# Performance work log

Hardware: AMD Instinct MI355X
Metric: run time of the kernel (lower is better)

Reference implementation:

```python
import jax, jax.numpy as jnp
from jax import lax
import numpy as np

L = 3          # seq_len == num_levels
B = 1
H = 180
W = 180
C = 128        # d_model
HEADS = 8
P = 4          # enc_num_points
DFF = 1024
DH = C // HEADS
HW = H * W
EPS = 1e-5


def _layer_norm(x, g, b):
    m = jnp.mean(x, axis=-1, keepdims=True)
    v = jnp.mean((x - m) ** 2, axis=-1, keepdims=True)
    return (x - m) * lax.rsqrt(v + EPS) * g + b


def _bilinear(v, x, y, h, w):
    # v: [B, heads, H*W, dh]; x, y: [B, heads, Q] in pixel coords (align_corners=False)
    x0 = jnp.floor(x)
    y0 = jnp.floor(y)
    out = jnp.zeros(v.shape[:2] + x.shape[2:] + (v.shape[-1],), v.dtype)
    for dx in (0, 1):
        for dy in (0, 1):
            cx = x0 + dx
            cy = y0 + dy
            wgt = (1.0 - jnp.abs(x - cx)) * (1.0 - jnp.abs(y - cy))
            valid = (cx >= 0) & (cx < w) & (cy >= 0) & (cy < h)
            idx = (jnp.clip(cy, 0, h - 1) * w + jnp.clip(cx, 0, w - 1)).astype(jnp.int32)
            g = jnp.take_along_axis(v, idx[..., None], axis=2)
            out = out + g * (wgt * valid.astype(v.dtype))[..., None]
    return out


def _forward(src_all, reference_points, spatial_shape, conv_w, conv_b,
             W_val, b_val, W_off, b_off, W_attn, b_attn, W_out, b_out,
             ln1_g, ln1_b, W1, b1, W2, b2, ln2_g, ln2_b):
    # ---- Query_generator: conv over cat(target, support) per temporal frame ----
    bev = jnp.transpose(src_all, (0, 1, 3, 2)).reshape(L, B, C, H, W)
    target = jnp.broadcast_to(bev[0][None], (L, B, C, H, W))
    x = jnp.concatenate([target, bev], axis=2).reshape(L * B, 2 * C, H, W)
    q = lax.conv_general_dilated(x, conv_w, (1, 1), 'SAME',
                                 dimension_numbers=('NCHW', 'OIHW', 'NCHW'))
    q = q + conv_b[None, :, None, None]
    queries = q.reshape(L, B, C, HW).transpose(0, 1, 3, 2)  # [L, B, HW, C]

    # ---- SeqMSDeformAttn ----
    key_tokens = jnp.transpose(src_all, (1, 0, 2, 3)).reshape(B, L * HW, C)
    value = (key_tokens @ W_val + b_val).reshape(B, L, HW, HEADS, DH)
    vflat = value.transpose(0, 1, 3, 2, 4)  # [B, L, heads, HW, dh]

    off = (queries @ W_off + b_off).reshape(L, B, HW, HEADS, P, 2)
    off = off.transpose(1, 2, 3, 0, 4, 5)  # [B, Lq, heads, L, P, 2]
    logits = (queries @ W_attn + b_attn).reshape(L, B, HW, HEADS, P)
    logits = logits.transpose(1, 2, 3, 0, 4)  # [B, Lq, heads, L, P]
    attn = jax.nn.softmax(logits.reshape(B, HW, HEADS, L * P), axis=-1)
    attn = attn.reshape(B, HW, HEADS, L, P)

    # offset normalizer = (W_l, H_l); locations normalized to [0,1]
    normalizer = spatial_shape[:, ::-1].astype(jnp.float32)  # [L, 2]
    locs = reference_points[:, :, None, :, None, :] + off / normalizer[None, None, None, :, None, :]

    out = jnp.zeros((B, HW, HEADS, DH), jnp.float32)
    for l in range(L):
        px = locs[:, :, :, l, :, 0] * W - 0.5  # [B, Lq, heads, P]
        py = locs[:, :, :, l, :, 1] * H - 0.5
        px = px.transpose(0, 2, 1, 3).reshape(B, HEADS, HW * P)
        py = py.transpose(0, 2, 1, 3).reshape(B, HEADS, HW * P)
        samp = _bilinear(vflat[:, l], px, py, H, W).reshape(B, HEADS, HW, P, DH)
        out = out + jnp.einsum('bhqpd,bqhp->bqhd', samp, attn[:, :, :, l, :])

    src2 = out.reshape(B, HW, C) @ W_out + b_out

    # ---- residual + norm + FFN (dropout = 0) ----
    src = _layer_norm(src_all[0] + src2, ln1_g, ln1_b)
    ffn = jax.nn.relu(src @ W1 + b1) @ W2 + b2
    return _layer_norm(src + ffn, ln2_g, ln2_b)


def setup_inputs() -> dict:
    key = jax.random.key(0)
    ks = jax.random.split(key, 12)
    s = 0.02
    return {
        'src_all': jax.random.normal(ks[0], (L, B, HW, C), jnp.float32),
        'reference_points': jax.random.uniform(ks[1], (B, HW, L, 2), dtype=jnp.float32),
        'spatial_shape': jnp.full((L, 2), 180, dtype=jnp.int32),
        'conv_w': jax.random.normal(ks[2], (C, 2 * C, 3, 3), jnp.float32) * s,
        'conv_b': jnp.zeros((C,), jnp.float32),
        'W_val': jax.random.normal(ks[3], (C, C), jnp.float32) * s,
        'b_val': jnp.zeros((C,), jnp.float32),
        'W_off': jax.random.normal(ks[4], (C, HEADS * P * 2), jnp.float32) * s,
        'b_off': jax.random.normal(ks[5], (HEADS * P * 2,), jnp.float32) * 0.1,
        'W_attn': jax.random.normal(ks[6], (C, HEADS * P), jnp.float32) * s,
        'b_attn': jnp.zeros((HEADS * P,), jnp.float32),
        'W_out': jax.random.normal(ks[7], (C, C), jnp.float32) * s,
        'b_out': jnp.zeros((C,), jnp.float32),
        'ln1_g': jnp.ones((C,), jnp.float32),
        'ln1_b': jnp.zeros((C,), jnp.float32),
        'W1': jax.random.normal(ks[8], (C, DFF), jnp.float32) * s,
        'b1': jnp.zeros((DFF,), jnp.float32),
        'W2': jax.random.normal(ks[9], (DFF, C), jnp.float32) * s,
        'b2': jnp.zeros((C,), jnp.float32),
        'ln2_g': jnp.ones((C,), jnp.float32),
        'ln2_b': jnp.zeros((C,), jnp.float32),
    }


def reference(src_all, reference_points, spatial_shape, conv_w, conv_b,
              W_val, b_val, W_off, b_off, W_attn, b_attn, W_out, b_out,
              ln1_g, ln1_b, W1, b1, W2, b2, ln2_g, ln2_b):
    return _forward(src_all, reference_points, spatial_shape, conv_w, conv_b,
                    W_val, b_val, W_off, b_off, W_attn, b_attn, W_out, b_out,
                    ln1_g, ln1_b, W1, b1, W2, b2, ln2_g, ln2_b)
```

## Files before the change

### kernel.cpp

```cpp
#include <hip/hip_runtime.h>

typedef unsigned short u16;
typedef unsigned int u32;

#define HDIM 180
#define HW 32400
#define CC 128

#define CAN_SRC   0
#define CAN_REF   12441600
#define CAN_CW    12636000
#define CAN_CB    12930912
#define CAN_WVAL  12931040
#define CAN_BVAL  12947424
#define CAN_WOFF  12947552
#define CAN_BOFF  12955744
#define CAN_WATTN 12955808
#define CAN_BATTN 12959904
#define CAN_WOUT  12959936
#define CAN_BOUT  12976320
#define CAN_LN1G  12976448
#define CAN_LN1B  12976576
#define CAN_W1    12976704
#define CAN_B1    13107776
#define CAN_W2    13108800
#define CAN_B2    13239872
#define CAN_LN2G  13240000
#define CAN_LN2B  13240128
#define CAN_TOTAL 13240256

typedef short short8 __attribute__((ext_vector_type(8)));
typedef float f32x4v __attribute__((ext_vector_type(4)));

__device__ __forceinline__ float bf2f(u16 v) { return __uint_as_float(((u32)v) << 16); }
__device__ __forceinline__ u16 f2bf(float f) {
    u32 x = __float_as_uint(f);
    return (u16)((x + 0x7FFFu + ((x >> 16) & 1u)) >> 16);
}
__device__ __forceinline__ void bf8_to_f(const uint4 v, float* o) {
    o[0] = __uint_as_float(v.x << 16); o[1] = __uint_as_float(v.x & 0xFFFF0000u);
    o[2] = __uint_as_float(v.y << 16); o[3] = __uint_as_float(v.y & 0xFFFF0000u);
    o[4] = __uint_as_float(v.z << 16); o[5] = __uint_as_float(v.z & 0xFFFF0000u);
    o[6] = __uint_as_float(v.w << 16); o[7] = __uint_as_float(v.w & 0xFFFF0000u);
}

struct PtrsZ { const void* p[20]; };

__global__ __launch_bounds__(256) void convert_z(PtrsZ ptrs, u16* __restrict__ out)
{
    const int offs[20] = {CAN_SRC, CAN_REF, CAN_CW, CAN_CB, CAN_WVAL, CAN_BVAL,
                          CAN_WOFF, CAN_BOFF, CAN_WATTN, CAN_BATTN, CAN_WOUT, CAN_BOUT,
                          CAN_LN1G, CAN_LN1B, CAN_W1, CAN_B1, CAN_W2, CAN_B2,
                          CAN_LN2G, CAN_LN2B};
    int gid = blockIdx.x * 256 + threadIdx.x;
    if (gid >= CAN_TOTAL) return;
    int t = 0;
    #pragma unroll
    for (int i = 1; i < 20; i++) t += (gid >= offs[i]) ? 1 : 0;
    int e = gid - offs[t];
    bool isb = (*(const u32*)ptrs.p[12]) == 0x3F803F80u;
    out[gid] = isb ? ((const u16*)ptrs.p[t])[e] : f2bf(((const float*)ptrs.p[t])[e]);
}

__global__ __launch_bounds__(256) void prep1_z(
    const u16* __restrict__ cw, const u16* __restrict__ wval, const u16* __restrict__ wout,
    const u16* __restrict__ woff, const u16* __restrict__ wattn,
    const u16* __restrict__ boff, const u16* __restrict__ battn,
    u16* __restrict__ wtbuf, u16* __restrict__ wvalT,
    u16* __restrict__ wcat, u16* __restrict__ b128, u16* __restrict__ woutT)
{
    int gid = blockIdx.x * 256 + threadIdx.x;
    if (gid < 294912) {
        int ci = gid & 127, co = (gid >> 7) & 127, rest = gid >> 14;
        int tap = rest % 9, half = rest / 9;
        wtbuf[gid] = cw[(size_t)co * 2304 + (half * 128 + ci) * 9 + tap];
    } else if (gid < 311296) {
        int e = gid - 294912;
        int k = e >> 7, n = e & 127;
        wvalT[n * 128 + k] = wval[e];
    } else if (gid < 327808) {
        int e = gid - 311296;
        if (e < 16384) {
            int n = e >> 7, k = e & 127;
            u16 v = 0;
            if (n < 64) v = woff[k * 64 + n];
            else if (n < 96) v = wattn[k * 32 + (n - 64)];
            wcat[n * 128 + k] = v;
        } else {
            int n = e - 16384;
            u16 v = 0;
            if (n < 64) v = boff[n]; else if (n < 96) v = battn[n - 64];
            b128[n] = v;
        }
    } else if (gid < 344192) {
        int e = gid - 327808;
        int k = e >> 7, n = e & 127;
        woutT[n * 128 + k] = wout[e];
    }
}

__global__ __launch_bounds__(256) void w12t_z(
    const u16* __restrict__ w1, const u16* __restrict__ w2,
    u16* __restrict__ w1t, u16* __restrict__ w2t)
{
    int gid = blockIdx.x * 256 + threadIdx.x;
    if (gid < 131072) {
        int k = gid >> 10, n = gid & 1023;
        w1t[(size_t)n * 128 + k] = w1[gid];
    } else if (gid < 262144) {
        int e = gid - 131072;
        int k = e >> 7, n = e & 127;
        w2t[(size_t)n * 1024 + k] = w2[e];
    }
}

template<bool OUT_BF16, bool RELU, bool RES>
__global__ __launch_bounds__(256) void gemm_z(
    const u16* __restrict__ A, const u16* __restrict__ W, const u16* __restrict__ bias,
    void* __restrict__ outp, const u16* __restrict__ res, int M, int N, int K)
{
    __shared__ float As[64][68];
    __shared__ float Bs[64][68];
    const int tid = threadIdx.x;
    const int tx = tid & 15, ty = tid >> 4;
    const int m0 = blockIdx.y * 64, n0 = blockIdx.x * 64;
    float acc[4][4] = {};

    for (int k0 = 0; k0 < K; k0 += 64) {
        __syncthreads();
        #pragma unroll
        for (int i = tid; i < 512; i += 256) {
            int row = i >> 3, part = i & 7;
            float f[8];
            if (m0 + row < M) {
                uint4 v = *(const uint4*)(A + (size_t)(m0 + row) * K + k0 + part * 8);
                bf8_to_f(v, f);
            } else {
                #pragma unroll
                for (int j = 0; j < 8; j++) f[j] = 0.f;
            }
            #pragma unroll
            for (int j = 0; j < 8; j++) As[part * 8 + j][row] = f[j];
        }
        #pragma unroll
        for (int i = tid; i < 512; i += 256) {
            int kr = i >> 3, np = i & 7;
            float f[8];
            uint4 v = *(const uint4*)(W + (size_t)(k0 + kr) * N + n0 + np * 8);
            bf8_to_f(v, f);
            #pragma unroll
            for (int j = 0; j < 8; j++) Bs[kr][np * 8 + j] = f[j];
        }
        __syncthreads();
        #pragma unroll 8
        for (int kk = 0; kk < 64; kk++) {
            float4 a = *(const float4*)&As[kk][ty * 4];
            float4 b = *(const float4*)&Bs[kk][tx * 4];
            float av[4] = {a.x, a.y, a.z, a.w};
            float bv[4] = {b.x, b.y, b.z, b.w};
            #pragma unroll
            for (int i = 0; i < 4; i++)
                #pragma unroll
                for (int j = 0; j < 4; j++)
                    acc[i][j] += av[i] * bv[j];
        }
    }

    #pragma unroll
    for (int i = 0; i < 4; i++) {
        int row = m0 + ty * 4 + i;
        if (row >= M) continue;
        #pragma unroll
        for (int j = 0; j < 4; j++) {
            int col = n0 + tx * 4 + j;
            float v = acc[i][j] + bf2f(bias[col]);
            if (RELU) v = v > 0.f ? v : 0.f;
            if (RES) v += bf2f(res[(size_t)row * N + col]);
            if (OUT_BF16) ((u16*)outp)[(size_t)row * N + col] = f2bf(v);
            else          ((float*)outp)[(size_t)row * N + col] = v;
        }
    }
}

__global__ __launch_bounds__(256) void conv_z(
    const u16* __restrict__ src, const u16* __restrict__ cw, const u16* __restrict__ cb,
    u16* __restrict__ queries)
{
    __shared__ float in_lds[8 * 6 * 22];
    __shared__ float w_lds[8 * 9 * 128];
    const int tid = threadIdx.x;
    const int wt = blockIdx.x, ht = blockIdx.y, l = blockIdx.z;
    const int h0 = ht * 4, w0 = wt * 20;
    const int cog = tid & 15, pxg = tid >> 4;
    const int pr = pxg >> 2, c0 = (pxg & 3) * 5;

    float acc[5][8] = {};

    for (int ch = 0; ch < 32; ch++) {
        const int ci0 = ch * 8;
        const int fsel = (ci0 < 128) ? 0 : l;
        const int cbase = ci0 & 127;
        __syncthreads();
        if (tid < 132) {
            int r = tid / 22, c = tid % 22;
            int gh = h0 - 1 + r, gw = w0 - 1 + c;
            float f[8];
            if (gh >= 0 && gh < HDIM && gw >= 0 && gw < HDIM) {
                uint4 v = *(const uint4*)(src + ((size_t)fsel * HW + gh * HDIM + gw) * CC + cbase);
                bf8_to_f(v, f);
            } else {
                #pragma unroll
                for (int j = 0; j < 8; j++) f[j] = 0.f;
            }
            #pragma unroll
            for (int j = 0; j < 8; j++) in_lds[j * 132 + r * 22 + c] = f[j];
        }
        for (int i = tid; i < 1152; i += 256) {
            int co = i & 127, part = i >> 7;
            uint4 v = *(const uint4*)(cw + (size_t)co * 2304 + ci0 * 9 + part * 8);
            float f[8]; bf8_to_f(v, f);
            #pragma unroll
            for (int j = 0; j < 8; j++) {
                int flat = part * 8 + j;
                int ci = flat / 9, k = flat % 9;
                w_lds[ci * 1152 + k * 128 + co] = f[j];
            }
        }
        __syncthreads();

        #pragma unroll
        for (int ci = 0; ci < 8; ci++) {
            float xv[3][7];
            #pragma unroll
            for (int r = 0; r < 3; r++)
                #pragma unroll
                for (int c = 0; c < 7; c++)
                    xv[r][c] = in_lds[ci * 132 + (pr + r) * 22 + (c0 + c)];
            const float* wbase = &w_lds[ci * 1152];
            #pragma unroll
            for (int j8 = 0; j8 < 8; j8++) {
                int co = cog + 16 * j8;
                float w_[9];
                #pragma unroll
                for (int k = 0; k < 9; k++) w_[k] = wbase[k * 128 + co];
                #pragma unroll
                for (int j = 0; j < 5; j++) {
                    acc[j][j8] += xv[0][j] * w_[0] + xv[0][j + 1] * w_[1] + xv[0][j + 2] * w_[2]
                                + xv[1][j] * w_[3] + xv[1][j + 1] * w_[4] + xv[1][j + 2] * w_[5]
                                + xv[2][j] * w_[6] + xv[2][j + 1] * w_[7] + xv[2][j + 2] * w_[8];
                }
            }
        }
    }

    float bias[8];
    #pragma unroll
    for (int j8 = 0; j8 < 8; j8++) bias[j8] = bf2f(cb[cog + 16 * j8]);
    #pragma unroll
    for (int j = 0; j < 5; j++) {
        int q = (h0 + pr) * HDIM + (w0 + c0 + j);
        u16* qp = queries + ((size_t)l * HW + q) * CC;
        #pragma unroll
        for (int j8 = 0; j8 < 8; j8++)
            qp[cog + 16 * j8] = f2bf(acc[j][j8] + bias[j8]);
    }
}

template<int MODE>
__global__ __launch_bounds__(256) void convh_z(
    const u16* __restrict__ src, const u16* __restrict__ wt, const u16* __restrict__ cb,
    f32x4v* __restrict__ q0, u16* __restrict__ queries)
{
    __shared__ uint4 Blds[2][2048];
    const int tid = threadIdx.x;
    const int wv = tid >> 6, ln = tid & 63;
    const int lo = ln & 15, hi = ln >> 4;
    const int l = (MODE == 1) ? blockIdx.y : 0;
    const int pix0 = blockIdx.x * 128 + wv * 32;
    const int pb0 = blockIdx.x * 8 + wv * 2;

    int ph[2], pc[2];
    #pragma unroll
    for (int s = 0; s < 2; s++) {
        int p = pix0 + s * 16 + lo;
        ph[s] = p / HDIM; pc[s] = p % HDIM;
    }

    f32x4v acc[2][8];
    if (MODE == 0) {
        #pragma unroll
        for (int s = 0; s < 2; s++)
            #pragma unroll
            for (int c = 0; c < 8; c++) acc[s][c] = (f32x4v){0.f, 0.f, 0.f, 0.f};
    } else {
        #pragma unroll
        for (int s = 0; s < 2; s++)
            #pragma unroll
            for (int c = 0; c < 8; c++)
                acc[s][c] = q0[((size_t)(pb0 + s) * 8 + c) * 64 + ln];
    }

    const u16* wthalf = wt + (MODE == 1 ? (size_t)9 * 16384 : 0);
    const u16* sbase  = src + (MODE == 1 ? (size_t)l * HW * CC : 0);

    const int sco = tid >> 1, spart = tid & 1;
    const int sc8 = sco >> 4, slo = sco & 15;

    {
        const uint4* g = (const uint4*)(wthalf + (size_t)sco * 128 + spart * 64);
        uint4 gr[8];
        #pragma unroll
        for (int i = 0; i < 8; i++) gr[i] = g[i];
        #pragma unroll
        for (int i = 0; i < 8; i++) {
            int k8 = spart * 8 + i;
            Blds[0][((k8 >> 2) * 8 + sc8) * 64 + (k8 & 3) * 16 + slo] = gr[i];
        }
    }
    __syncthreads();

    for (int t = 0; t < 9; t++) {
        const int cur = t & 1;

        uint4 gr[8];
        if (t < 8) {
            const uint4* g = (const uint4*)(wthalf + (size_t)(t + 1) * 16384 +
                                            (size_t)sco * 128 + spart * 64);
            #pragma unroll
            for (int i = 0; i < 8; i++) gr[i] = g[i];
        }

        const int dy = t / 3 - 1, dx = t % 3 - 1;
        const int sh0 = ph[0] + dy, sc0 = pc[0] + dx;
        const int sh1 = ph[1] + dy, sc1 = pc[1] + dx;
        const bool v0 = (sh0 >= 0) && (sh0 < HDIM) && (sc0 >= 0) && (sc0 < HDIM);
        const bool v1 = (sh1 >= 0) && (sh1 < HDIM) && (sc1 >= 0) && (sc1 < HDIM);
        const u16* arow0 = sbase + (size_t)(sh0 * HDIM + sc0) * CC;
        const u16* arow1 = sbase + (size_t)(sh1 * HDIM + sc1) * CC;

        #pragma unroll
        for (int kc = 0; kc < 4; kc++) {
            short8 a0 = {}, a1 = {};
            if (v0) a0 = *(const short8*)(arow0 + kc * 32 + hi * 8);
            if (v1) a1 = *(const short8*)(arow1 + kc * 32 + hi * 8);
            #pragma unroll
            for (int c = 0; c < 8; c++) {
                short8 b = ((const short8*)&Blds[cur][0])[(kc * 8 + c) * 64 + ln];
                acc[0][c] = __builtin_amdgcn_mfma_f32_16x16x32_bf16(a0, b, acc[0][c], 0, 0, 0);
                acc[1][c] = __builtin_amdgcn_mfma_f32_16x16x32_bf16(a1, b, acc[1][c], 0, 0, 0);
            }
        }

        if (t < 8) {
            #pragma unroll
            for (int i = 0; i < 8; i++) {
                int k8 = spart * 8 + i;
                Blds[cur ^ 1][((k8 >> 2) * 8 + sc8) * 64 + (k8 & 3) * 16 + slo] = gr[i];
            }
        }
        __syncthreads();
    }

    if (MODE == 0) {
        #pragma unroll
        for (int s = 0; s < 2; s++)
            #pragma unroll
            for (int c = 0; c < 8; c++)
                q0[((size_t)(pb0 + s) * 8 + c) * 64 + ln] = acc[s][c];
    } else {
        #pragma unroll
        for (int s = 0; s < 2; s++) {
            #pragma unroll
            for (int c = 0; c < 8; c++) {
                float bv = bf2f(cb[c * 16 + lo]);
                #pragma unroll
                for (int r = 0; r < 4; r++) {
                    int pr = pix0 + s * 16 + hi * 4 + r;
                    if (pr < HW)
                        queries[((size_t)l * HW + pr) * CC + c * 16 + lo] =
                            f2bf(acc[s][c][r] + bv);
                }
            }
        }
    }
}

template<int OMODE, bool RELU, bool RES, bool LN>
__global__ __launch_bounds__(256) void gemmm_z(
    const u16* __restrict__ A, const u16* __restrict__ WT, const u16* __restrict__ bias,
    void* __restrict__ outp, const u16* __restrict__ res,
    const u16* __restrict__ lng, const u16* __restrict__ lnb,
    int M, int K, int ldc, int ncols)
{
    __shared__ u16 Blds[128 * 136];
    const int tid = threadIdx.x;
    const int wv = tid >> 6, ln = tid & 63;
    const int lo = ln & 15, hi = ln >> 4;
    const int m0 = blockIdx.y * 64, n0 = blockIdx.x * 128;
    const int row = m0 + wv * 16 + lo;
    const u16* arow = A + (size_t)row * K;

    f32x4v acc[8] = {};

    for (int ks = 0; ks < K; ks += 128) {
        __syncthreads();
        {
            int n = tid >> 1, part = tid & 1;
            const uint4* g = (const uint4*)(WT + (size_t)(n0 + n) * K + ks + part * 64);
            uint4* d = (uint4*)&Blds[n * 136 + part * 64];
            #pragma unroll
            for (int i = 0; i < 8; i++) d[i] = g[i];
        }
        __syncthreads();
        #pragma unroll
        for (int kc = 0; kc < 4; kc++) {
            short8 a = *(const short8*)(arow + ks + kc * 32 + hi * 8);
            #pragma unroll
            for (int c = 0; c < 8; c++) {
                short8 b = *(const short8*)&Blds[(c * 16 + lo) * 136 + kc * 32 + hi * 8];
                acc[c] = __builtin_amdgcn_mfma_f32_16x16x32_bf16(a, b, acc[c], 0, 0, 0);
            }
        }
    }

    #pragma unroll
    for (int r = 0; r < 4; r++) {
        int orow = m0 + wv * 16 + hi * 4 + r;
        if (orow >= M) continue;
        float vv[8];
        #pragma unroll
        for (int c = 0; c < 8; c++) {
            int col = n0 + c * 16 + lo;
            float v = 0.f;
            if (col < ncols) {
                v = acc[c][r] + bf2f(bias[col]);
                if (RELU) v = v > 0.f ? v : 0.f;
                if (RES) v += bf2f(res[(size_t)orow * ldc + col]);
            }
            vv[c] = v;
        }
        if (LN) {
            float s1 = 0.f;
            #pragma unroll
            for (int c = 0; c < 8; c++) s1 += vv[c];
            #pragma unroll
            for (int o = 8; o; o >>= 1) s1 += __shfl_xor(s1, o, 64);
            float mean = s1 * (1.f / 128.f);
            float s2 = 0.f;
            #pragma unroll
            for (int c = 0; c < 8; c++) { float d = vv[c] - mean; s2 += d * d; }
            #pragma unroll
            for (int o = 8; o; o >>= 1) s2 += __shfl_xor(s2, o, 64);
            float rr = rsqrtf(s2 * (1.f / 128.f) + 1e-5f);
            #pragma unroll
            for (int c = 0; c < 8; c++) {
                int col = n0 + c * 16 + lo;
                vv[c] = (vv[c] - mean) * rr * bf2f(lng[col]) + bf2f(lnb[col]);
            }
        }
        #pragma unroll
        for (int c = 0; c < 8; c++) {
            int col = n0 + c * 16 + lo;
            if (col >= ncols) continue;
            if (OMODE == 0)
                ((float*)outp)[(size_t)orow * ldc + col] = vv[c];
            else
                ((u16*)outp)[(size_t)orow * ldc + col] = f2bf(vv[c]);
        }
    }
}

__global__ __launch_bounds__(256, 4) void sample3_z(
    const u16* __restrict__ value, const float* __restrict__ proj,
    const float* __restrict__ ref, u16* __restrict__ outp)
{
    const int tid = threadIdx.x;
    const int q = blockIdx.x * 16 + (tid >> 4);
    const int head = tid & 7;
    const int phv = (tid >> 3) & 1;
    if (q >= HW) return;

    float lg[12];
    #pragma unroll
    for (int l = 0; l < 3; l++) {
        float4 v = *(const float4*)(proj + (size_t)(l * HW + q) * 96 + 64 + head * 4);
        lg[l * 4 + 0] = v.x; lg[l * 4 + 1] = v.y; lg[l * 4 + 2] = v.z; lg[l * 4 + 3] = v.w;
    }
    float m = lg[0];
    #pragma unroll
    for (int i = 1; i < 12; i++) m = fmaxf(m, lg[i]);
    float w12[12], sum = 0.f;
    #pragma unroll
    for (int i = 0; i < 12; i++) { w12[i] = __expf(lg[i] - m); sum += w12[i]; }
    float inv = 1.f / sum;

    float acc[16] = {};
    #pragma unroll
    for (int l = 0; l < 3; l++) {
        float rx = ref[(size_t)(q * 3 + l) * 2 + 0] * 180.f - 0.5f;
        float ry = ref[(size_t)(q * 3 + l) * 2 + 1] * 180.f - 0.5f;
        float4 o = *(const float4*)(proj + (size_t)(l * HW + q) * 96 + head * 8 + phv * 4);
        float ox[2] = {o.x, o.z};
        float oy[2] = {o.y, o.w};
        #pragma unroll
        for (int pp = 0; pp < 2; pp++) {
            int p = phv * 2 + pp;
            float px = rx + ox[pp];
            float py = ry + oy[pp];
            float x0f = floorf(px), y0f = floorf(py);
            int x0 = (int)x0f, y0 = (int)y0f;
            float fx = px - x0f, fy = py - y0f;
            float a = w12[l * 4 + p] * inv;
            #pragma unroll
            for (int dy = 0; dy < 2; dy++) {
                int cy = y0 + dy;
                float wy = (dy ? fy : 1.f - fy) * a;
                wy = (cy >= 0 && cy < HDIM) ? wy : 0.f;
                int cyc = min(max(cy, 0), HDIM - 1);
                #pragma unroll
                for (int dx = 0; dx < 2; dx++) {
                    int cx = x0 + dx;
                    float wq = (dx ? fx : 1.f - fx) * wy;
                    wq = (cx >= 0 && cx < HDIM) ? wq : 0.f;
                    int cxc = min(max(cx, 0), HDIM - 1);
                    const uint4* vp = (const uint4*)(value +
                        (((size_t)l * HW + cyc * HDIM + cxc) * CC + head * 16));
                    uint4 va = vp[0], vb = vp[1];
                    float f[8];
                    bf8_to_f(va, f);
                    #pragma unroll
                    for (int d = 0; d < 8; d++) acc[d] += wq * f[d];
                    bf8_to_f(vb, f);
                    #pragma unroll
                    for (int d = 0; d < 8; d++) acc[8 + d] += wq * f[d];
                }
            }
        }
    }
    #pragma unroll
    for (int d = 0; d < 16; d++) acc[d] += __shfl_xor(acc[d], 8, 64);
    if (phv == 0) {
        u16 pack[16];
        #pragma unroll
        for (int d = 0; d < 16; d++) pack[d] = f2bf(acc[d]);
        uint4* op = (uint4*)(outp + (size_t)q * CC + head * 16);
        op[0] = ((uint4*)pack)[0];
        op[1] = ((uint4*)pack)[1];
    }
}

__global__ __launch_bounds__(256) void sample_z(
    const u16* __restrict__ value, const u16* __restrict__ queries,
    const u16* __restrict__ woff, const u16* __restrict__ boff,
    const u16* __restrict__ wattn, const u16* __restrict__ battn,
    const float* __restrict__ ref, u16* __restrict__ outp)
{
    __shared__ u16 w_lds[128 * 96];
    __shared__ float bias_lds[96];
    const int tid = threadIdx.x;

    for (int i = tid; i < 128 * 96; i += 256) {
        int k = i / 96, c = i % 96;
        w_lds[i] = (c < 64) ? woff[k * 64 + c] : wattn[k * 32 + (c - 64)];
    }
    if (tid < 96) bias_lds[tid] = bf2f(tid < 64 ? boff[tid] : battn[tid - 64]);
    __syncthreads();

    int q = blockIdx.x * 32 + (tid >> 3);
    int head = tid & 7;
    if (q >= HW) return;

    float og[3][8], lg[12];
    #pragma unroll
    for (int l = 0; l < 3; l++) {
        const u16* qr = queries + ((size_t)l * HW + q) * CC;
        float a12[12] = {};
        #pragma unroll
        for (int kc = 0; kc < 16; kc++) {
            float f[8];
            bf8_to_f(*(const uint4*)(qr + kc * 8), f);
            #pragma unroll
            for (int j = 0; j < 8; j++) {
                const u16* wr = &w_lds[(kc * 8 + j) * 96];
                #pragma unroll
                for (int c = 0; c < 8; c++) a12[c] += f[j] * bf2f(wr[head * 8 + c]);
                #pragma unroll
                for (int c = 0; c < 4; c++) a12[8 + c] += f[j] * bf2f(wr[64 + head * 4 + c]);
            }
        }
        #pragma unroll
        for (int c = 0; c < 8; c++) og[l][c] = a12[c] + bias_lds[head * 8 + c];
        #pragma unroll
        for (int c = 0; c < 4; c++) lg[l * 4 + c] = a12[8 + c] + bias_lds[64 + head * 4 + c];
    }

    float m = lg[0];
    #pragma unroll
    for (int i = 1; i < 12; i++) m = fmaxf(m, lg[i]);
    float w12[12], sum = 0.f;
    #pragma unroll
    for (int i = 0; i < 12; i++) { w12[i] = __expf(lg[i] - m); sum += w12[i]; }
    float inv = 1.f / sum;

    float acc[16] = {};
    #pragma unroll
    for (int l = 0; l < 3; l++) {
        float rx = ref[(size_t)(q * 3 + l) * 2 + 0];
        float ry = ref[(size_t)(q * 3 + l) * 2 + 1];
        #pragma unroll
        for (int p = 0; p < 4; p++) {
            float px = rx * 180.f + og[l][p * 2 + 0] - 0.5f;
            float py = ry * 180.f + og[l][p * 2 + 1] - 0.5f;
            float x0f = floorf(px), y0f = floorf(py);
            int x0 = (int)x0f, y0 = (int)y0f;
            float fx = px - x0f, fy = py - y0f;
            float a = w12[l * 4 + p] * inv;
            #pragma unroll
            for (int dy = 0; dy < 2; dy++) {
                int cy = y0 + dy;
                if (cy < 0 || cy >= HDIM) continue;
                #pragma unroll
                for (int dx = 0; dx < 2; dx++) {
                    int cx = x0 + dx;
                    if (cx < 0 || cx >= HDIM) continue;
                    float wq = a * ((dx ? fx : 1.f - fx) * (dy ? fy : 1.f - fy));
                    const uint4* vp = (const uint4*)(value + (((size_t)l * HW + cy * HDIM + cx) * CC + head * 16));
                    uint4 va = vp[0], vb = vp[1];
                    float f[8];
                    bf8_to_f(va, f);
                    #pragma unroll
                    for (int d = 0; d < 8; d++) acc[d] += wq * f[d];
                    bf8_to_f(vb, f);
                    #pragma unroll
                    for (int d = 0; d < 8; d++) acc[8 + d] += wq * f[d];
                }
            }
        }
    }
    u16 pack[16];
    #pragma unroll
    for (int d = 0; d < 16; d++) pack[d] = f2bf(acc[d]);
    uint4* op = (uint4*)(outp + (size_t)q * CC + head * 16);
    op[0] = ((uint4*)pack)[0];
    op[1] = ((uint4*)pack)[1];
}

__global__ __launch_bounds__(256) void ln_z(
    u16* __restrict__ x, const u16* __restrict__ g, const u16* __restrict__ b, int M)
{
    int row = blockIdx.x * 4 + (threadIdx.x >> 6);
    int lane = threadIdx.x & 63;
    if (row >= M) return;
    u16* xr = x + (size_t)row * 128;
    float v0 = bf2f(xr[lane]), v1 = bf2f(xr[lane + 64]);
    float s = v0 + v1;
    #pragma unroll
    for (int o = 32; o; o >>= 1) s += __shfl_xor(s, o, 64);
    float mean = s * (1.f / 128.f);
    float d0 = v0 - mean, d1 = v1 - mean;
    float vs = d0 * d0 + d1 * d1;
    #pragma unroll
    for (int o = 32; o; o >>= 1) vs += __shfl_xor(vs, o, 64);
    float r = rsqrtf(vs * (1.f / 128.f) + 1e-5f);
    xr[lane]      = f2bf(d0 * r * bf2f(g[lane])      + bf2f(b[lane]));
    xr[lane + 64] = f2bf(d1 * r * bf2f(g[lane + 64]) + bf2f(b[lane + 64]));
}

__global__ __launch_bounds__(256) void ln32_z(
    float* __restrict__ x, const u16* __restrict__ g, const u16* __restrict__ b, int M)
{
    int row = blockIdx.x * 4 + (threadIdx.x >> 6);
    int lane = threadIdx.x & 63;
    if (row >= M) return;
    float* xr = x + (size_t)row * 128;
    float v0 = xr[lane], v1 = xr[lane + 64];
    float s = v0 + v1;
    #pragma unroll
    for (int o = 32; o; o >>= 1) s += __shfl_xor(s, o, 64);
    float mean = s * (1.f / 128.f);
    float d0 = v0 - mean, d1 = v1 - mean;
    float vs = d0 * d0 + d1 * d1;
    #pragma unroll
    for (int o = 32; o; o >>= 1) vs += __shfl_xor(vs, o, 64);
    float r = rsqrtf(vs * (1.f / 128.f) + 1e-5f);
    xr[lane]      = d0 * r * bf2f(g[lane])      + bf2f(b[lane]);
    xr[lane + 64] = d1 * r * bf2f(g[lane + 64]) + bf2f(b[lane + 64]);
}

extern "C" void kernel_launch(void* const* d_in, const int* in_sizes, int n_in,
                              void* d_out, int out_size, void* d_ws, size_t ws_size,
                              hipStream_t stream)
{
    char* ws = (char*)d_ws;
    u16* canon   = (u16*)ws;
    u16* value   = (u16*)(ws + 26480512);
    u16* queries = (u16*)(ws + 51363712);
    u16* src     = (u16*)(ws + 26480512);
    float* dout  = (float*)d_out;

    const size_t PROJ_OFF = 76246912;
    const size_t PROJ_END = PROJ_OFF + (size_t)3 * HW * 96 * 4;
    const bool big = ws_size >= PROJ_END;
    float* proj  = (float*)(ws + PROJ_OFF);
    u16* wtbuf   = (u16*)(ws + PROJ_OFF);
    f32x4v* q0   = (f32x4v*)(ws + PROJ_OFF + 1048576);
    u16* out_s   = big ? (u16*)(ws + 51363712) : (u16*)(ws + 76246912);
    u16* hidden  = (u16*)(ws + 51363712);

    u16* WvalT = (u16*)(ws + 51363712);
    u16* W1T   = (u16*)(ws + 34774912);
    u16* W2T   = (u16*)(ws + 35037056);
    u16* wcatT = (u16*)d_out;
    u16* b128  = (u16*)d_out + 16384;
    u16* WoutT = (u16*)d_out + 32768;

    int i_cw = 2;
    while (i_cw < n_in - 17 && in_sizes[i_cw] != 294912) i_cw++;
    if (i_cw >= n_in - 17) i_cw = 3;

    PtrsZ ptrs;
    ptrs.p[0] = d_in[0];
    ptrs.p[1] = d_in[1];
    for (int i = 0; i < 18; i++) ptrs.p[2 + i] = d_in[i_cw + i];

    const u16* csrc  = canon + CAN_SRC;
    const u16* ccw   = canon + CAN_CW;
    const u16* ccb   = canon + CAN_CB;
    const u16* cWval = canon + CAN_WVAL,  *cbval = canon + CAN_BVAL;
    const u16* cWoff = canon + CAN_WOFF,  *cboff = canon + CAN_BOFF;
    const u16* cWatt = canon + CAN_WATTN, *cbatt = canon + CAN_BATTN;
    const u16* cWout = canon + CAN_WOUT,  *cbout = canon + CAN_BOUT;
    const u16* cg1   = canon + CAN_LN1G,  *cb1n  = canon + CAN_LN1B;
    const u16* cW1   = canon + CAN_W1,    *cbf1  = canon + CAN_B1;
    const u16* cW2   = canon + CAN_W2,    *cbf2  = canon + CAN_B2;
    const u16* cg2   = canon + CAN_LN2G,  *cb2n  = canon + CAN_LN2B;

    convert_z<<<dim3((CAN_TOTAL + 255) / 256), 256, 0, stream>>>(ptrs, canon);

    const int M3 = 3 * HW, M1 = HW;

    if (big) {
        prep1_z<<<dim3((344192 + 255) / 256), 256, 0, stream>>>(
            ccw, cWval, cWout, cWoff, cWatt, cboff, cbatt,
            wtbuf, WvalT, wcatT, b128, WoutT);
        gemmm_z<1, false, false, false><<<dim3(1, 1519), 256, 0, stream>>>(
            csrc, WvalT, cbval, value, nullptr, nullptr, nullptr, M3, 128, 128, 128);
        convh_z<0><<<dim3((HW + 127) / 128, 1), 256, 0, stream>>>(
            csrc, wtbuf, ccb, q0, queries);
        convh_z<1><<<dim3((HW + 127) / 128, 3), 256, 0, stream>>>(
            csrc, wtbuf, ccb, q0, queries);
        gemmm_z<0, false, false, false><<<dim3(1, 1519), 256, 0, stream>>>(
            queries, wcatT, b128, proj, nullptr, nullptr, nullptr, M3, 128, 96, 96);
        sample3_z<<<dim3((HW + 15) / 16), 256, 0, stream>>>(
            value, proj, (const float*)d_in[1], out_s);
        w12t_z<<<dim3(1024), 256, 0, stream>>>(cW1, cW2, W1T, W2T);
        gemmm_z<1, false, true, true><<<dim3(1, 507), 256, 0, stream>>>(
            out_s, WoutT, cbout, src, csrc, cg1, cb1n, M1, 128, 128, 128);
        for (int sblk = 0; sblk < 2; sblk++) {
            const u16* srow = src + (size_t)sblk * 16200 * 128;
            float* drow = dout + (size_t)sblk * 16200 * 128;
            gemmm_z<1, true, false, false><<<dim3(8, 254), 256, 0, stream>>>(
                srow, W1T, cbf1, hidden, nullptr, nullptr, nullptr, 16200, 128, 1024, 1024);
            gemmm_z<0, false, true, true><<<dim3(1, 254), 256, 0, stream>>>(
                hidden, W2T, cbf2, drow, srow, cg2, cb2n, 16200, 1024, 128, 128);
        }
    } else {
        u16* out_f = (u16*)(ws + 76246912);
        u16* hid_f = (u16*)(ws + 51363712);
        gemm_z<true, false, false><<<dim3(2, 1519), 256, 0, stream>>>(
            csrc, cWval, cbval, value, nullptr, M3, 128, 128);
        conv_z<<<dim3(9, 45, 3), 256, 0, stream>>>(csrc, ccw, ccb, queries);
        sample_z<<<dim3(1013), 256, 0, stream>>>(
            value, queries, cWoff, cboff, cWatt, cbatt, (const float*)d_in[1], out_f);
        gemm_z<true, false, true><<<dim3(2, 507), 256, 0, stream>>>(
            out_f, cWout, cbout, src, csrc, M1, 128, 128);
        ln_z<<<dim3(8100), 256, 0, stream>>>(src, cg1, cb1n, M1);
        for (int sblk = 0; sblk < 4; sblk++) {
            const u16* srow = src + (size_t)sblk * 8100 * 128;
            float* drow = dout + (size_t)sblk * 8100 * 128;
            gemm_z<true, true, false><<<dim3(16, 127), 256, 0, stream>>>(
                srow, cW1, cbf1, hid_f, nullptr, 8100, 1024, 128);
            gemm_z<false, false, true><<<dim3(2, 127), 256, 0, stream>>>(
                hid_f, cW2, cbf2, drow, srow, 8100, 128, 1024);
        }
        ln32_z<<<dim3(8100), 256, 0, stream>>>(dout, cg2, cb2n, M1);
    }
}
```

Before: 597.5 us.

## Fold offset/attention projection weights into the query conv weights

Precomputes the product of the 3x3 conv weights with the concatenated offset/attention projection matrix, plus a folded bias, so the conv kernels write the 96-wide projection directly. This removes the separate projection GEMM and the bf16 queries intermediate, and narrows the conv output from 128 to 96 channels. In exchange it adds a small weight-fold kernel that runs every call, and it changes rounding because the folded weights are stored in bf16.

```diff
diff --git a/kernel.cpp b/kernel.cpp
--- a/kernel.cpp
+++ b/kernel.cpp
@@ -63,39 +63,44 @@
 }
 
 __global__ __launch_bounds__(256) void prep1_z(
-    const u16* __restrict__ cw, const u16* __restrict__ wval, const u16* __restrict__ wout,
-    const u16* __restrict__ woff, const u16* __restrict__ wattn,
-    const u16* __restrict__ boff, const u16* __restrict__ battn,
-    u16* __restrict__ wtbuf, u16* __restrict__ wvalT,
-    u16* __restrict__ wcat, u16* __restrict__ b128, u16* __restrict__ woutT)
+    const u16* __restrict__ wval, const u16* __restrict__ wout,
+    u16* __restrict__ wvalT, u16* __restrict__ woutT)
 {
     int gid = blockIdx.x * 256 + threadIdx.x;
-    if (gid < 294912) {
-        int ci = gid & 127, co = (gid >> 7) & 127, rest = gid >> 14;
-        int tap = rest % 9, half = rest / 9;
-        wtbuf[gid] = cw[(size_t)co * 2304 + (half * 128 + ci) * 9 + tap];
-    } else if (gid < 311296) {
-        int e = gid - 294912;
-        int k = e >> 7, n = e & 127;
-        wvalT[n * 128 + k] = wval[e];
-    } else if (gid < 327808) {
-        int e = gid - 311296;
-        if (e < 16384) {
-            int n = e >> 7, k = e & 127;
-            u16 v = 0;
-            if (n < 64) v = woff[k * 64 + n];
-            else if (n < 96) v = wattn[k * 32 + (n - 64)];
-            wcat[n * 128 + k] = v;
-        } else {
-            int n = e - 16384;
-            u16 v = 0;
-            if (n < 64) v = boff[n]; else if (n < 96) v = battn[n - 64];
-            b128[n] = v;
-        }
-    } else if (gid < 344192) {
-        int e = gid - 327808;
+    if (gid < 16384) {
+        int k = gid >> 7, n = gid & 127;
+        wvalT[n * 128 + k] = wval[gid];
+    } else if (gid < 32768) {
+        int e = gid - 16384;
         int k = e >> 7, n = e & 127;
         woutT[n * 128 + k] = wout[e];
+    }
+}
+
+__global__ __launch_bounds__(256) void wfold_z(
+    const u16* __restrict__ cw, const u16* __restrict__ woff, const u16* __restrict__ wattn,
+    const u16* __restrict__ boff, const u16* __restrict__ battn, const u16* __restrict__ cb,
+    u16* __restrict__ wf, float* __restrict__ pb)
+{
+    int gid = blockIdx.x * 256 + threadIdx.x;
+    if (gid < 221184) {
+        int ci = gid & 127;
+        int n  = (gid >> 7) % 96;
+        int rest = gid / 12288;
+        int t = rest % 9, h = rest / 9;
+        float acc = 0.f;
+        for (int co = 0; co < 128; co++) {
+            float wc  = bf2f(cw[(size_t)co * 2304 + (h * 128 + ci) * 9 + t]);
+            float cat = bf2f(n < 64 ? woff[co * 64 + n] : wattn[co * 32 + (n - 64)]);
+            acc += wc * cat;
+        }
+        wf[((size_t)(h * 9 + t) * 96 + n) * 128 + ci] = f2bf(acc);
+    } else if (gid < 221280) {
+        int n = gid - 221184;
+        float acc = bf2f(n < 64 ? boff[n] : battn[n - 64]);
+        for (int k = 0; k < 128; k++)
+            acc += bf2f(cb[k]) * bf2f(n < 64 ? woff[k * 64 + n] : wattn[k * 32 + (n - 64)]);
+        pb[n] = acc;
     }
 }
 
@@ -268,10 +273,10 @@
 
 template<int MODE>
 __global__ __launch_bounds__(256) void convh_z(
-    const u16* __restrict__ src, const u16* __restrict__ wt, const u16* __restrict__ cb,
-    f32x4v* __restrict__ q0, u16* __restrict__ queries)
-{
-    __shared__ uint4 Blds[2][2048];
+    const u16* __restrict__ src, const u16* __restrict__ wf, const float* __restrict__ pb,
+    f32x4v* __restrict__ p0, float* __restrict__ proj)
+{
+    __shared__ uint4 Blds[2][1536];
     const int tid = threadIdx.x;
     const int wv = tid >> 6, ln = tid & 63;
     const int lo = ln & 15, hi = ln >> 4;
@@ -286,35 +291,35 @@
         ph[s] = p / HDIM; pc[s] = p % HDIM;
     }
 
-    f32x4v acc[2][8];
+    f32x4v acc[2][6];
     if (MODE == 0) {
         #pragma unroll
         for (int s = 0; s < 2; s++)
             #pragma unroll
-            for (int c = 0; c < 8; c++) acc[s][c] = (f32x4v){0.f, 0.f, 0.f, 0.f};
+            for (int c = 0; c < 6; c++) acc[s][c] = (f32x4v){0.f, 0.f, 0.f, 0.f};
     } else {
         #pragma unroll
         for (int s = 0; s < 2; s++)
             #pragma unroll
-            for (int c = 0; c < 8; c++)
-                acc[s][c] = q0[((size_t)(pb0 + s) * 8 + c) * 64 + ln];
-    }
-
-    const u16* wthalf = wt + (MODE == 1 ? (size_t)9 * 16384 : 0);
+            for (int c = 0; c < 6; c++)
+                acc[s][c] = p0[((size_t)(pb0 + s) * 6 + c) * 64 + ln];
+    }
+
+    const u16* wfhalf = wf + (MODE == 1 ? (size_t)9 * 12288 : 0);
     const u16* sbase  = src + (MODE == 1 ? (size_t)l * HW * CC : 0);
 
-    const int sco = tid >> 1, spart = tid & 1;
-    const int sc8 = sco >> 4, slo = sco & 15;
-
-    {
-        const uint4* g = (const uint4*)(wthalf + (size_t)sco * 128 + spart * 64);
+    const int sn = tid >> 1, spart = tid & 1;
+    const int sc6 = sn >> 4, slo = sn & 15;
+
+    if (tid < 192) {
+        const uint4* g = (const uint4*)(wfhalf + (size_t)sn * 128 + spart * 64);
         uint4 gr[8];
         #pragma unroll
         for (int i = 0; i < 8; i++) gr[i] = g[i];
         #pragma unroll
         for (int i = 0; i < 8; i++) {
             int k8 = spart * 8 + i;
-            Blds[0][((k8 >> 2) * 8 + sc8) * 64 + (k8 & 3) * 16 + slo] = gr[i];
+            Blds[0][((k8 >> 2) * 6 + sc6) * 64 + (k8 & 3) * 16 + slo] = gr[i];
         }
     }
     __syncthreads();
@@ -323,9 +328,9 @@
         const int cur = t & 1;
 
         uint4 gr[8];
-        if (t < 8) {
-            const uint4* g = (const uint4*)(wthalf + (size_t)(t + 1) * 16384 +
-                                            (size_t)sco * 128 + spart * 64);
+        if (t < 8 && tid < 192) {
+            const uint4* g = (const uint4*)(wfhalf + (size_t)(t + 1) * 12288 +
+                                            (size_t)sn * 128 + spart * 64);
             #pragma unroll
             for (int i = 0; i < 8; i++) gr[i] = g[i];
         }
@@ -344,18 +349,18 @@
             if (v0) a0 = *(const short8*)(arow0 + kc * 32 + hi * 8);
             if (v1) a1 = *(const short8*)(arow1 + kc * 32 + hi * 8);
             #pragma unroll
-            for (int c = 0; c < 8; c++) {
-                short8 b = ((const short8*)&Blds[cur][0])[(kc * 8 + c) * 64 + ln];
+            for (int c = 0; c < 6; c++) {
+                short8 b = ((const short8*)&Blds[cur][0])[(kc * 6 + c) * 64 + ln];
                 acc[0][c] = __builtin_amdgcn_mfma_f32_16x16x32_bf16(a0, b, acc[0][c], 0, 0, 0);
                 acc[1][c] = __builtin_amdgcn_mfma_f32_16x16x32_bf16(a1, b, acc[1][c], 0, 0, 0);
             }
         }
 
-        if (t < 8) {
+        if (t < 8 && tid < 192) {
             #pragma unroll
             for (int i = 0; i < 8; i++) {
                 int k8 = spart * 8 + i;
-                Blds[cur ^ 1][((k8 >> 2) * 8 + sc8) * 64 + (k8 & 3) * 16 + slo] = gr[i];
+                Blds[cur ^ 1][((k8 >> 2) * 6 + sc6) * 64 + (k8 & 3) * 16 + slo] = gr[i];
             }
         }
         __syncthreads();
@@ -365,20 +370,19 @@
         #pragma unroll
         for (int s = 0; s < 2; s++)
             #pragma unroll
-            for (int c = 0; c < 8; c++)
-                q0[((size_t)(pb0 + s) * 8 + c) * 64 + ln] = acc[s][c];
+            for (int c = 0; c < 6; c++)
+                p0[((size_t)(pb0 + s) * 6 + c) * 64 + ln] = acc[s][c];
     } else {
         #pragma unroll
         for (int s = 0; s < 2; s++) {
             #pragma unroll
-            for (int c = 0; c < 8; c++) {
-                float bv = bf2f(cb[c * 16 + lo]);
+            for (int c = 0; c < 6; c++) {
+                float bv = pb[c * 16 + lo];
                 #pragma unroll
                 for (int r = 0; r < 4; r++) {
                     int pr = pix0 + s * 16 + hi * 4 + r;
                     if (pr < HW)
-                        queries[((size_t)l * HW + pr) * CC + c * 16 + lo] =
-                            f2bf(acc[s][c][r] + bv);
+                        proj[((size_t)l * HW + pr) * 96 + c * 16 + lo] = acc[s][c][r] + bv;
                 }
             }
         }
@@ -694,7 +698,6 @@
     char* ws = (char*)d_ws;
     u16* canon   = (u16*)ws;
     u16* value   = (u16*)(ws + 26480512);
-    u16* queries = (u16*)(ws + 51363712);
     u16* src     = (u16*)(ws + 26480512);
     float* dout  = (float*)d_out;
 
@@ -702,17 +705,17 @@
     const size_t PROJ_END = PROJ_OFF + (size_t)3 * HW * 96 * 4;
     const bool big = ws_size >= PROJ_END;
     float* proj  = (float*)(ws + PROJ_OFF);
-    u16* wtbuf   = (u16*)(ws + PROJ_OFF);
-    f32x4v* q0   = (f32x4v*)(ws + PROJ_OFF + 1048576);
-    u16* out_s   = big ? (u16*)(ws + 51363712) : (u16*)(ws + 76246912);
+
+    u16* WvalT = (u16*)(ws + 51363712);
+    u16* wfold = (u16*)(ws + 51363712 + 65536);
+    f32x4v* p0 = (f32x4v*)(ws + 51363712 + 1048576);
+    u16* out_s   = (u16*)(ws + 51363712);
     u16* hidden  = (u16*)(ws + 51363712);
 
-    u16* WvalT = (u16*)(ws + 51363712);
     u16* W1T   = (u16*)(ws + 34774912);
     u16* W2T   = (u16*)(ws + 35037056);
-    u16* wcatT = (u16*)d_out;
-    u16* b128  = (u16*)d_out + 16384;
-    u16* WoutT = (u16*)d_out + 32768;
+    u16* WoutT = (u16*)d_out;
+    float* pbv = (float*)((u16*)d_out + 32768);
 
     int i_cw = 2;
     while (i_cw < n_in - 17 && in_sizes[i_cw] != 294912) i_cw++;
@@ -740,17 +743,15 @@
     const int M3 = 3 * HW, M1 = HW;
 
     if (big) {
-        prep1_z<<<dim3((344192 + 255) / 256), 256, 0, stream>>>(
-            ccw, cWval, cWout, cWoff, cWatt, cboff, cbatt,
-            wtbuf, WvalT, wcatT, b128, WoutT);
+        prep1_z<<<dim3(128), 256, 0, stream>>>(cWval, cWout, WvalT, WoutT);
+        wfold_z<<<dim3((221280 + 255) / 256), 256, 0, stream>>>(
+            ccw, cWoff, cWatt, cboff, cbatt, ccb, wfold, pbv);
         gemmm_z<1, false, false, false><<<dim3(1, 1519), 256, 0, stream>>>(
             csrc, WvalT, cbval, value, nullptr, nullptr, nullptr, M3, 128, 128, 128);
         convh_z<0><<<dim3((HW + 127) / 128, 1), 256, 0, stream>>>(
-            csrc, wtbuf, ccb, q0, queries);
+            csrc, wfold, pbv, p0, proj);
         convh_z<1><<<dim3((HW + 127) / 128, 3), 256, 0, stream>>>(
-            csrc, wtbuf, ccb, q0, queries);
-        gemmm_z<0, false, false, false><<<dim3(1, 1519), 256, 0, stream>>>(
-            queries, wcatT, b128, proj, nullptr, nullptr, nullptr, M3, 128, 96, 96);
+            csrc, wfold, pbv, p0, proj);
         sample3_z<<<dim3((HW + 15) / 16), 256, 0, stream>>>(
             value, proj, (const float*)d_in[1], out_s);
         w12t_z<<<dim3(1024), 256, 0, stream>>>(cW1, cW2, W1T, W2T);
@@ -765,6 +766,7 @@
                 hidden, W2T, cbf2, drow, srow, cg2, cb2n, 16200, 1024, 128, 128);
         }
     } else {
+        u16* queries = (u16*)(ws + 51363712);
         u16* out_f = (u16*)(ws + 76246912);
         u16* hid_f = (u16*)(ws + 51363712);
         gemm_z<true, false, false><<<dim3(2, 1519), 256, 0, stream>>>(
```

Measured after the change: 621.9 us. 1.04x slower.
